# Performance work log

Hardware: AMD Instinct MI355X
Metric: run time of the kernel (lower is better)

Reference implementation:

```python
import jax, jax.numpy as jnp
import numpy as np

E = 8      # n_routed_experts
TOPK = 2
D = 768    # hidden_dim
F = 3072   # routed_expert_inter_dim (== shared_expert_inter_dim)


def setup_inputs() -> dict:
    key = jax.random.key(0)
    ks = jax.random.split(key, 11)
    s = 0.02
    return {
        "x": jax.random.normal(ks[0], (2, 64, 64, D), dtype=jnp.float32),
        "gate_w": jax.random.normal(ks[1], (E, D), dtype=jnp.float32),          # Gate.weight (torch randn init)
        "w1": jax.random.normal(ks[2], (E, F, D), dtype=jnp.float32) * s,       # Expert.fc1.weight per expert
        "b1": jax.random.normal(ks[3], (E, F), dtype=jnp.float32) * s,
        "w2": jax.random.normal(ks[4], (E, D, F), dtype=jnp.float32) * s,       # Expert.fc2.weight per expert
        "b2": jax.random.normal(ks[5], (E, D), dtype=jnp.float32) * s,
        "ws1": jax.random.normal(ks[6], (F, D), dtype=jnp.float32) * s,         # shared GeluMLP fc1
        "bs1": jax.random.normal(ks[7], (F,), dtype=jnp.float32) * s,
        "ws2": jax.random.normal(ks[8], (D, F), dtype=jnp.float32) * s,         # shared GeluMLP fc2
        "bs2": jax.random.normal(ks[9], (D,), dtype=jnp.float32) * s,
    }


def _gelu(v):
    return jax.nn.gelu(v, approximate=False)  # torch nn.GELU default = exact erf


def reference(x, gate_w, w1, b1, w2, b2, ws1, bs1, ws2, bs2):
    B, H, W, Dh = x.shape
    xf = x.reshape(-1, Dh)                                  # [T, D]
    T = xf.shape[0]

    # Gate: softmax over expert logits, top-k, renormalize
    scores = jax.nn.softmax(xf @ gate_w.T, axis=-1)         # [T, E]
    vals, idx = jax.lax.top_k(scores, TOPK)                 # [T, K]
    vals = vals / jnp.sum(vals, axis=-1, keepdims=True)

    # Dense combine weights: 0 for unselected experts (faithful to scatter-add)
    cw = jnp.zeros((T, E), dtype=xf.dtype).at[
        jnp.arange(T)[:, None], idx
    ].add(vals)                                             # [T, E]

    # Routed experts: small fixed structural loop over E experts
    out = jnp.zeros_like(xf)
    for e in range(E):
        h = _gelu(xf @ w1[e].T + b1[e])                     # [T, F]
        y = h @ w2[e].T + b2[e]                             # [T, D]
        out = out + y * cw[:, e:e + 1]

    # Shared expert (GeluMLP) applied to all tokens
    shared = _gelu(xf @ ws1.T + bs1) @ ws2.T + bs2          # [T, D]

    return (out + shared).reshape(B, H, W, Dh)
```

## Files before the change

kernel.cpp:

```cpp
#include <hip/hip_runtime.h>
#include <hip/hip_bf16.h>

#define T_TOK 8192
#define E_EXP 8
#define DDIM  768
#define FDIM  3072

typedef _Float16 f16x8 __attribute__((ext_vector_type(8)));
typedef _Float16 f16x4 __attribute__((ext_vector_type(4)));
typedef float    f32x4 __attribute__((ext_vector_type(4)));

static const size_t XH_OFF   = 0;
static const size_t W1H_OFF  = 12582912;
static const size_t W2H_OFF  = 50331648;
static const size_t WS1H_OFF = 88080384;
static const size_t WS2H_OFF = 92798976;
static const size_t H_OFF    = 97517568;
static const size_t ROWS_OFF = 198180864;
static const size_t RW_OFF   = 198246400;
static const size_t TIDX_OFF = 198311936;
static const size_t TW_OFF   = 198377472;
static const size_t CNT_OFF  = 198443008;
static const size_t BASE_OFF = 198443264;
static const size_t CUR_OFF  = 198443520;
static const size_t WS_NEED  = 198443776;

__global__ void cvt_f32_f16(const float* __restrict__ src, _Float16* __restrict__ dst, int n4) {
    int i = blockIdx.x * blockDim.x + threadIdx.x;
    if (i >= n4) return;
    float4 v = ((const float4*)src)[i];
    f16x4 o = { (_Float16)v.x, (_Float16)v.y, (_Float16)v.z, (_Float16)v.w };
    *(f16x4*)(dst + 4 * (size_t)i) = o;
}

__global__ void gate_kernel(const float* __restrict__ x, const float* __restrict__ gw,
                            int* __restrict__ tidx, float* __restrict__ tw) {
    int wave = threadIdx.x >> 6;
    int lane = threadIdx.x & 63;
    int t = blockIdx.x * 4 + wave;
    const float4* xv = (const float4*)(x + (size_t)t * DDIM);
    float p[E_EXP];
#pragma unroll
    for (int e = 0; e < E_EXP; e++) p[e] = 0.f;
    for (int i = lane; i < DDIM / 4; i += 64) {
        float4 xv4 = xv[i];
#pragma unroll
        for (int e = 0; e < E_EXP; e++) {
            float4 g = ((const float4*)(gw + (size_t)e * DDIM))[i];
            p[e] += xv4.x * g.x + xv4.y * g.y + xv4.z * g.z + xv4.w * g.w;
        }
    }
#pragma unroll
    for (int e = 0; e < E_EXP; e++) {
#pragma unroll
        for (int off = 32; off; off >>= 1) p[e] += __shfl_xor(p[e], off);
    }
    if (lane == 0) {
        int i0 = 0;
#pragma unroll
        for (int e = 1; e < E_EXP; e++) if (p[e] > p[i0]) i0 = e;
        int i1 = (i0 == 0) ? 1 : 0;
#pragma unroll
        for (int e = 0; e < E_EXP; e++) {
            if (e == i0) continue;
            if (p[e] > p[i1]) i1 = e;
        }
        float d  = p[i1] - p[i0];
        float e1 = expf(d);
        float w0 = 1.f / (1.f + e1);
        float w1 = 1.f - w0;
        tidx[2 * t]     = i0;  tw[2 * t]     = w0;
        tidx[2 * t + 1] = i1;  tw[2 * t + 1] = w1;
    }
}

__global__ void count_kernel(const int* __restrict__ tidx, int* __restrict__ cnt,
                             int* __restrict__ base, int* __restrict__ cur) {
    int c[E_EXP];
#pragma unroll
    for (int e = 0; e < E_EXP; e++) c[e] = 0;
    for (int i = threadIdx.x; i < 2 * T_TOK; i += 1024) {
        int e = tidx[i];
#pragma unroll
        for (int k = 0; k < E_EXP; k++) c[k] += (e == k) ? 1 : 0;
    }
#pragma unroll
    for (int e = 0; e < E_EXP; e++) {
#pragma unroll
        for (int off = 32; off; off >>= 1) c[e] += __shfl_xor(c[e], off);
    }
    __shared__ int wsum[16][E_EXP];
    int lane = threadIdx.x & 63, wave = threadIdx.x >> 6;
    if (lane == 0) {
#pragma unroll
        for (int e = 0; e < E_EXP; e++) wsum[wave][e] = c[e];
    }
    __syncthreads();
    if (threadIdx.x == 0) {
        int acc = 0;
        for (int e = 0; e < E_EXP; e++) {
            int s = 0;
            for (int w = 0; w < 16; w++) s += wsum[w][e];
            cnt[e] = s; base[e] = acc; cur[e] = acc; acc += s;
        }
    }
}

__global__ void scatter_kernel(const int* __restrict__ tidx, const float* __restrict__ tw,
                               int* __restrict__ cur, int* __restrict__ rowsIdx,
                               float* __restrict__ rw) {
    int t = blockIdx.x * 256 + threadIdx.x;
    int lane = threadIdx.x & 63, wave = threadIdx.x >> 6;
    unsigned long long lt = (lane == 63) ? 0x7FFFFFFFFFFFFFFFull
                                         : ((1ull << lane) - 1ull) | 0ull;
    lt = ((unsigned long long)1 << lane) - 1ull;
    __shared__ int wcnt[8][E_EXP];
    __shared__ int wpre[8][E_EXP];
    __shared__ int bbase[E_EXP];

    int myE[2], myR[2];
#pragma unroll
    for (int k = 0; k < 2; k++) {
        int e = tidx[2 * t + k];
        myE[k] = e;
        int vw = wave * 2 + k;
        int rank = 0;
#pragma unroll
        for (int ee = 0; ee < E_EXP; ee++) {
            unsigned long long m = __ballot(e == ee);
            if (e == ee) rank = __builtin_popcountll(m & lt);
            if (lane == 0) wcnt[vw][ee] = __builtin_popcountll(m);
        }
        myR[k] = rank;
    }
    __syncthreads();
    if (threadIdx.x < E_EXP) {
        int e = threadIdx.x, acc = 0;
#pragma unroll
        for (int vw = 0; vw < 8; vw++) { wpre[vw][e] = acc; acc += wcnt[vw][e]; }
        bbase[e] = atomicAdd(&cur[e], acc);
    }
    __syncthreads();
#pragma unroll
    for (int k = 0; k < 2; k++) {
        int e = myE[k];
        int slot = bbase[e] + wpre[wave * 2 + k][e] + myR[k];
        rowsIdx[slot] = t;
        rw[slot] = tw[2 * t + k];
    }
}

#define FC1S 0
#define FC2S 1
#define FC1R 2
#define FC2R 3

template <int MODE>
__global__ __launch_bounds__(256, 2) void gemm_kernel(
    const _Float16* __restrict__ Abase,
    const _Float16* __restrict__ Wbase,
    const float* __restrict__ biasBase,
    _Float16* __restrict__ h,
    float* __restrict__ out,
    const int* __restrict__ cnt, const int* __restrict__ base,
    const int* __restrict__ rowsIdx, const float* __restrict__ rw)
{
    constexpr int K = (MODE == FC1S || MODE == FC1R) ? DDIM : FDIM;
    constexpr int N = (MODE == FC1S || MODE == FC1R) ? FDIM : DDIM;
    constexpr bool ROUTED = (MODE == FC1R || MODE == FC2R);

    int m0, mEnd;
    const _Float16* W;
    const float* bias;
    if constexpr (ROUTED) {
        int bx = blockIdx.x, accb = 0, expert = -1, rb = 0;
#pragma unroll
        for (int e = 0; e < E_EXP; e++) {
            int nb = (cnt[e] + 127) >> 7;
            if (expert < 0 && bx < accb + nb) { expert = e; rb = bx - accb; }
            accb += nb;
        }
        if (expert < 0) return;
        m0   = base[expert] + rb * 128;
        mEnd = base[expert] + cnt[expert];
        W    = Wbase + (size_t)expert * N * K;
        bias = biasBase + (size_t)expert * N;
    } else {
        m0 = blockIdx.x * 128;
        mEnd = T_TOK;
        W = Wbase;
        bias = biasBase;
    }
    int n0 = blockIdx.y * 128;

    __shared__ __align__(16) _Float16 As[128 * 72];
    __shared__ __align__(16) _Float16 Bs[128 * 72];

    int tid  = threadIdx.x;
    int lane = tid & 63;
    int wid  = tid >> 6;
    int wm   = wid >> 1, wn = wid & 1;
    int m16  = lane & 15, q = lane >> 4;

    f32x4 acc[4][4];
#pragma unroll
    for (int i = 0; i < 4; i++)
#pragma unroll
        for (int j = 0; j < 4; j++) acc[i][j] = f32x4{0.f, 0.f, 0.f, 0.f};

    int arowg[4];
#pragma unroll
    for (int tse = 0; tse < 4; tse++) {
        int s = tid + tse * 256;
        int row = s >> 3;
        int pr = m0 + row;
        bool valid = pr < mEnd;
        int ar;
        if constexpr (MODE == FC1R) ar = valid ? rowsIdx[pr] : 0;
        else                        ar = pr;
        arowg[tse] = valid ? ar : -1;
    }

    for (int k0 = 0; k0 < K; k0 += 64) {
#pragma unroll
        for (int tse = 0; tse < 4; tse++) {
            int s = tid + tse * 256;
            int row = s >> 3, cs = s & 7;
            int4 v = make_int4(0, 0, 0, 0);
            int ar = arowg[tse];
            if (ar >= 0) v = *(const int4*)(Abase + (size_t)ar * K + k0 + cs * 8);
            *(int4*)(As + row * 72 + cs * 8) = v;
        }
#pragma unroll
        for (int tse = 0; tse < 4; tse++) {
            int s = tid + tse * 256;
            int row = s >> 3, cs = s & 7;
            int4 v = *(const int4*)(W + (size_t)(n0 + row) * K + k0 + cs * 8);
            *(int4*)(Bs + row * 72 + cs * 8) = v;
        }
        __syncthreads();
#pragma unroll
        for (int ks = 0; ks < 2; ks++) {
            f16x8 af[4], bf[4];
#pragma unroll
            for (int i = 0; i < 4; i++)
                af[i] = *(const f16x8*)(As + (wm * 64 + i * 16 + m16) * 72 + ks * 32 + q * 8);
#pragma unroll
            for (int j = 0; j < 4; j++)
                bf[j] = *(const f16x8*)(Bs + (wn * 64 + j * 16 + m16) * 72 + ks * 32 + q * 8);
#pragma unroll
            for (int i = 0; i < 4; i++)
#pragma unroll
                for (int j = 0; j < 4; j++)
                    acc[i][j] = __builtin_amdgcn_mfma_f32_16x16x32_f16(af[i], bf[j], acc[i][j], 0, 0, 0);
        }
        __syncthreads();
    }

    float biasv[4];
#pragma unroll
    for (int j = 0; j < 4; j++) biasv[j] = bias[n0 + wn * 64 + j * 16 + m16];

#pragma unroll
    for (int i = 0; i < 4; i++) {
#pragma unroll
        for (int r = 0; r < 4; r++) {
            int rowp = m0 + wm * 64 + i * 16 + q * 4 + r;
            if (rowp >= mEnd) continue;
            int tok = 0; float wgt = 0.f;
            if constexpr (MODE == FC2R) { tok = rowsIdx[rowp]; wgt = rw[rowp]; }
#pragma unroll
            for (int j = 0; j < 4; j++) {
                int col = n0 + wn * 64 + j * 16 + m16;
                float v = acc[i][j][r] + biasv[j];
                if constexpr (MODE == FC1S || MODE == FC1R) {
                    v = 0.5f * v * (1.f + erff(v * 0.70710678118f));
                    h[(size_t)rowp * FDIM + col] = (_Float16)v;
                } else if constexpr (MODE == FC2S) {
                    out[(size_t)rowp * DDIM + col] = v;
                } else {
                    atomicAdd(&out[(size_t)tok * DDIM + col], v * wgt);
                }
            }
        }
    }
}

extern "C" void kernel_launch(void* const* d_in, const int* in_sizes, int n_in,
                              void* d_out, int out_size, void* d_ws, size_t ws_size,
                              hipStream_t stream) {
    const float* x   = (const float*)d_in[0];
    const float* gw  = (const float*)d_in[1];
    const float* w1  = (const float*)d_in[2];
    const float* b1  = (const float*)d_in[3];
    const float* w2  = (const float*)d_in[4];
    const float* b2  = (const float*)d_in[5];
    const float* ws1 = (const float*)d_in[6];
    const float* bs1 = (const float*)d_in[7];
    const float* ws2 = (const float*)d_in[8];
    const float* bs2 = (const float*)d_in[9];
    float* out = (float*)d_out;
    char* ws = (char*)d_ws;
    if (ws_size < WS_NEED) return;

    _Float16* xh   = (_Float16*)(ws + XH_OFF);
    _Float16* w1h  = (_Float16*)(ws + W1H_OFF);
    _Float16* w2h  = (_Float16*)(ws + W2H_OFF);
    _Float16* ws1h = (_Float16*)(ws + WS1H_OFF);
    _Float16* ws2h = (_Float16*)(ws + WS2H_OFF);
    _Float16* h    = (_Float16*)(ws + H_OFF);
    int*   rowsIdx = (int*)(ws + ROWS_OFF);
    float* rw      = (float*)(ws + RW_OFF);
    int*   tidx    = (int*)(ws + TIDX_OFF);
    float* tw      = (float*)(ws + TW_OFF);
    int*   cnt     = (int*)(ws + CNT_OFF);
    int*   base    = (int*)(ws + BASE_OFF);
    int*   cur     = (int*)(ws + CUR_OFF);

    cvt_f32_f16<<<6144,  256, 0, stream>>>(x,   xh,   1572864);
    cvt_f32_f16<<<18432, 256, 0, stream>>>(w1,  w1h,  4718592);
    cvt_f32_f16<<<18432, 256, 0, stream>>>(w2,  w2h,  4718592);
    cvt_f32_f16<<<2304,  256, 0, stream>>>(ws1, ws1h, 589824);
    cvt_f32_f16<<<2304,  256, 0, stream>>>(ws2, ws2h, 589824);

    gate_kernel<<<2048, 256, 0, stream>>>(x, gw, tidx, tw);
    count_kernel<<<1, 1024, 0, stream>>>(tidx, cnt, base, cur);
    scatter_kernel<<<32, 256, 0, stream>>>(tidx, tw, cur, rowsIdx, rw);

    gemm_kernel<FC1S><<<dim3(64, 24),  256, 0, stream>>>(xh, ws1h, bs1, h, out, cnt, base, rowsIdx, rw);
    gemm_kernel<FC2S><<<dim3(64, 6),   256, 0, stream>>>(h,  ws2h, bs2, h, out, cnt, base, rowsIdx, rw);
    gemm_kernel<FC1R><<<dim3(136, 24), 256, 0, stream>>>(xh, w1h,  b1,  h, out, cnt, base, rowsIdx, rw);
    gemm_kernel<FC2R><<<dim3(136, 6),  256, 0, stream>>>(h,  w2h,  b2,  h, out, cnt, base, rowsIdx, rw);
}
```

Baseline: 720.1 us.

## Replace FC2 routed atomic scatter-add with slot-wise fp16 buffer and combine kernel

The routed FC2 epilogue now writes weighted per-slot outputs as fp16 into a buffer that reuses the w1h region, instead of doing float atomicAdd into the token rows. Scatter also records each token's two slots, and a new combine kernel gathers both slot rows and adds them into the shared-expert output. This removes atomic contention and random atomic traffic. In exchange it adds an extra pass over the output, plus fp16 rounding of the routed contributions.

```diff
diff --git a/kernel.cpp b/kernel.cpp
--- a/kernel.cpp
+++ b/kernel.cpp
@@ -12,6 +12,7 @@
 
 static const size_t XH_OFF   = 0;
 static const size_t W1H_OFF  = 12582912;
+static const size_t Y_OFF    = W1H_OFF;
 static const size_t W2H_OFF  = 50331648;
 static const size_t WS1H_OFF = 88080384;
 static const size_t WS2H_OFF = 92798976;
@@ -23,7 +24,8 @@
 static const size_t CNT_OFF  = 198443008;
 static const size_t BASE_OFF = 198443264;
 static const size_t CUR_OFF  = 198443520;
-static const size_t WS_NEED  = 198443776;
+static const size_t TSLOT_OFF= 198443776;
+static const size_t WS_NEED  = 198509312;
 
 __global__ void cvt_f32_f16(const float* __restrict__ src, _Float16* __restrict__ dst, int n4) {
     int i = blockIdx.x * blockDim.x + threadIdx.x;
@@ -108,12 +110,10 @@
 
 __global__ void scatter_kernel(const int* __restrict__ tidx, const float* __restrict__ tw,
                                int* __restrict__ cur, int* __restrict__ rowsIdx,
-                               float* __restrict__ rw) {
+                               float* __restrict__ rw, int* __restrict__ tslot) {
     int t = blockIdx.x * 256 + threadIdx.x;
     int lane = threadIdx.x & 63, wave = threadIdx.x >> 6;
-    unsigned long long lt = (lane == 63) ? 0x7FFFFFFFFFFFFFFFull
-                                         : ((1ull << lane) - 1ull) | 0ull;
-    lt = ((unsigned long long)1 << lane) - 1ull;
+    unsigned long long lt = ((unsigned long long)1 << lane) - 1ull;
     __shared__ int wcnt[8][E_EXP];
     __shared__ int wpre[8][E_EXP];
     __shared__ int bbase[E_EXP];
@@ -147,7 +147,30 @@
         int slot = bbase[e] + wpre[wave * 2 + k][e] + myR[k];
         rowsIdx[slot] = t;
         rw[slot] = tw[2 * t + k];
-    }
+        tslot[2 * t + k] = slot;
+    }
+}
+
+__global__ void combine_kernel(const _Float16* __restrict__ y,
+                               const int* __restrict__ tslot,
+                               float* __restrict__ out) {
+    int idx = blockIdx.x * 256 + threadIdx.x;
+    int t = idx / (DDIM / 8);
+    int c = (idx % (DDIM / 8)) * 8;
+    int s0 = tslot[2 * t], s1 = tslot[2 * t + 1];
+    f16x8 a = *(const f16x8*)(y + (size_t)s0 * DDIM + c);
+    f16x8 b = *(const f16x8*)(y + (size_t)s1 * DDIM + c);
+    float4* o = (float4*)(out + (size_t)t * DDIM + c);
+    float4 o0 = o[0], o1 = o[1];
+    o0.x += (float)a[0] + (float)b[0];
+    o0.y += (float)a[1] + (float)b[1];
+    o0.z += (float)a[2] + (float)b[2];
+    o0.w += (float)a[3] + (float)b[3];
+    o1.x += (float)a[4] + (float)b[4];
+    o1.y += (float)a[5] + (float)b[5];
+    o1.z += (float)a[6] + (float)b[6];
+    o1.w += (float)a[7] + (float)b[7];
+    o[0] = o0; o[1] = o1;
 }
 
 #define FC1S 0
@@ -267,8 +290,8 @@
         for (int r = 0; r < 4; r++) {
             int rowp = m0 + wm * 64 + i * 16 + q * 4 + r;
             if (rowp >= mEnd) continue;
-            int tok = 0; float wgt = 0.f;
-            if constexpr (MODE == FC2R) { tok = rowsIdx[rowp]; wgt = rw[rowp]; }
+            float wgt = 0.f;
+            if constexpr (MODE == FC2R) wgt = rw[rowp];
 #pragma unroll
             for (int j = 0; j < 4; j++) {
                 int col = n0 + wn * 64 + j * 16 + m16;
@@ -279,7 +302,7 @@
                 } else if constexpr (MODE == FC2S) {
                     out[(size_t)rowp * DDIM + col] = v;
                 } else {
-                    atomicAdd(&out[(size_t)tok * DDIM + col], v * wgt);
+                    h[(size_t)rowp * DDIM + col] = (_Float16)(v * wgt);
                 }
             }
         }
@@ -305,6 +328,7 @@
 
     _Float16* xh   = (_Float16*)(ws + XH_OFF);
     _Float16* w1h  = (_Float16*)(ws + W1H_OFF);
+    _Float16* yb   = (_Float16*)(ws + Y_OFF);
     _Float16* w2h  = (_Float16*)(ws + W2H_OFF);
     _Float16* ws1h = (_Float16*)(ws + WS1H_OFF);
     _Float16* ws2h = (_Float16*)(ws + WS2H_OFF);
@@ -316,6 +340,7 @@
     int*   cnt     = (int*)(ws + CNT_OFF);
     int*   base    = (int*)(ws + BASE_OFF);
     int*   cur     = (int*)(ws + CUR_OFF);
+    int*   tslot   = (int*)(ws + TSLOT_OFF);
 
     cvt_f32_f16<<<6144,  256, 0, stream>>>(x,   xh,   1572864);
     cvt_f32_f16<<<18432, 256, 0, stream>>>(w1,  w1h,  4718592);
@@ -325,10 +350,12 @@
 
     gate_kernel<<<2048, 256, 0, stream>>>(x, gw, tidx, tw);
     count_kernel<<<1, 1024, 0, stream>>>(tidx, cnt, base, cur);
-    scatter_kernel<<<32, 256, 0, stream>>>(tidx, tw, cur, rowsIdx, rw);
+    scatter_kernel<<<32, 256, 0, stream>>>(tidx, tw, cur, rowsIdx, rw, tslot);
 
     gemm_kernel<FC1S><<<dim3(64, 24),  256, 0, stream>>>(xh, ws1h, bs1, h, out, cnt, base, rowsIdx, rw);
     gemm_kernel<FC2S><<<dim3(64, 6),   256, 0, stream>>>(h,  ws2h, bs2, h, out, cnt, base, rowsIdx, rw);
     gemm_kernel<FC1R><<<dim3(136, 24), 256, 0, stream>>>(xh, w1h,  b1,  h, out, cnt, base, rowsIdx, rw);
-    gemm_kernel<FC2R><<<dim3(136, 6),  256, 0, stream>>>(h,  w2h,  b2,  h, out, cnt, base, rowsIdx, rw);
-}
+    gemm_kernel<FC2R><<<dim3(136, 6),  256, 0, stream>>>(h,  w2h,  b2,  yb, out, cnt, base, rowsIdx, rw);
+
+    combine_kernel<<<3072, 256, 0, stream>>>(yb, tslot, out);
+}
```

New measurement: 714.7 us. No clear change (-0.8%).
